# Performance work log

Hardware: AMD Instinct MI355X
Metric: run time of the kernel (lower is better)

## Reference

```python
import jax, jax.numpy as jnp
import numpy as np

HEAD, D_MODEL, D_KV = 16, 1024, 64
B, NQ, NK = 2, 2048, 2048


def setup_inputs() -> dict:
    key = jax.random.key(0)
    ks = jax.random.split(key, 10)
    s = 1.0 / np.sqrt(D_MODEL)
    return {
        "queries": jax.random.normal(ks[0], (B, NQ, D_MODEL), jnp.float32),
        "keys": jax.random.normal(ks[1], (B, NK, D_MODEL), jnp.float32),
        "values": jax.random.normal(ks[2], (B, NK, D_MODEL), jnp.float32),
        "group_prob": jax.random.uniform(ks[3], (B, 1, NQ, NK), jnp.float32),
        "attention_mask": jnp.ones((B, NK), jnp.int32),
        "Wq": jax.random.normal(ks[4], (D_MODEL, HEAD * D_KV), jnp.float32) * s,
        "bq": jnp.zeros((HEAD * D_KV,), jnp.float32),
        "Wk": jax.random.normal(ks[5], (D_MODEL, HEAD * D_KV), jnp.float32) * s,
        "bk": jnp.zeros((HEAD * D_KV,), jnp.float32),
        "Wv": jax.random.normal(ks[6], (D_MODEL, HEAD * D_KV), jnp.float32) * s,
        "bv": jnp.zeros((HEAD * D_KV,), jnp.float32),
    }


def reference(queries, keys, values, group_prob, attention_mask, Wq, bq, Wk, bk, Wv, bv):
    b_s, nq, _ = queries.shape
    nk = keys.shape[1]
    # projections -> [b, h, n, d]
    q = (queries @ Wq + bq).reshape(b_s, nq, HEAD, D_KV).transpose(0, 2, 1, 3)
    k = (keys @ Wk + bk).reshape(b_s, nk, HEAD, D_KV).transpose(0, 2, 1, 3)
    v = (values @ Wv + bv).reshape(b_s, nk, HEAD, D_KV).transpose(0, 2, 1, 3)
    att = jnp.einsum("bhqd,bhkd->bhqk", q, k) / np.sqrt(D_KV).astype(np.float32)
    # NOTE: original uses non-in-place `att.masked_fill(...)` and discards the
    # result, so attention_mask has NO effect on the computation. Replicated.
    att = jax.nn.softmax(att, axis=-1)
    att = att * group_prob  # post-softmax group gating, broadcast over heads
    out = jnp.einsum("bhqk,bhkd->bhqd", att, v)
    return out.transpose(0, 2, 1, 3).reshape(b_s, nq, D_MODEL)
```

## Files before the change

### kernel.cpp

```cpp
#include <hip/hip_runtime.h>
#include <hip/hip_bf16.h>
#include <cstdint>

typedef unsigned short ushort_t;
typedef __attribute__((ext_vector_type(8))) short short8;
typedef __attribute__((ext_vector_type(4))) float floatx4;
typedef __attribute__((ext_vector_type(4))) unsigned short ushort4_t;

#define H_   16
#define DKV_ 64
#define DM_  1024
#define B_   2
#define NQ_  2048
#define NK_  2048

__device__ __forceinline__ unsigned short f2bf(float f) {
  union { float f; unsigned int u; } v; v.f = f;
  unsigned int u = v.u;
  return (unsigned short)((u + 0x7fffu + ((u >> 16) & 1u)) >> 16);
}

__device__ __forceinline__ float fexp2(float x) { return __builtin_amdgcn_exp2f(x); }
__device__ __forceinline__ float frcp(float x)  { return __builtin_amdgcn_rcpf(x); }

__device__ __forceinline__ floatx4 mfma16(short8 a, short8 b, floatx4 c) {
  return __builtin_amdgcn_mfma_f32_16x16x32_bf16(a, b, c, 0, 0, 0);
}

__device__ __forceinline__ void gload_lds16(const ushort_t* g, ushort_t* l) {
  __builtin_amdgcn_global_load_lds(
      (const __attribute__((address_space(1))) void*)g,
      (__attribute__((address_space(3))) void*)l, 16, 0, 0);
}

__global__ __launch_bounds__(256) void cast_x_kernel(
    const float* __restrict__ q, const float* __restrict__ k,
    const float* __restrict__ v, ushort_t* __restrict__ dst)
{
  const int t = blockIdx.y;
  const float* src = (t == 0) ? q : (t == 1) ? k : v;
  ushort_t* d = dst + (size_t)t * 4096 * 1024;
  const int gid = blockIdx.x * 256 + threadIdx.x;
  #pragma unroll
  for (int u = 0; u < 8; u++) {
    const int i4 = u * 131072 + gid;
    floatx4 f = ((const floatx4*)src)[i4];
    ushort4_t o;
    #pragma unroll
    for (int e = 0; e < 4; e++) o[e] = f2bf(f[e]);
    *(ushort4_t*)&d[(size_t)i4 * 4] = o;
  }
}

__global__ __launch_bounds__(256) void cast_wt_kernel(
    const float* __restrict__ Wq, const float* __restrict__ Wk,
    const float* __restrict__ Wv, ushort_t* __restrict__ WtAll)
{
  __shared__ ushort_t tile[32][33];
  const int t = blockIdx.z;
  const float* W = (t == 0) ? Wq : (t == 1) ? Wk : Wv;
  ushort_t* Wt = WtAll + (size_t)t * 1024 * 1024;
  const int n0 = blockIdx.x * 32, k0 = blockIdx.y * 32;
  const int tid = threadIdx.x, r = tid >> 3, c4 = (tid & 7) * 4;
  floatx4 f = *(const floatx4*)&W[(size_t)(k0 + r) * 1024 + n0 + c4];
  #pragma unroll
  for (int e = 0; e < 4; e++) tile[r][c4 + e] = f2bf(f[e]);
  __syncthreads();
  ushort4_t o;
  #pragma unroll
  for (int e = 0; e < 4; e++) o[e] = tile[c4 + e][r];
  *(ushort4_t*)&Wt[(size_t)(n0 + r) * 1024 + k0 + c4] = o;
}

__global__ __launch_bounds__(256, 2) void proj_kernel2(
    const ushort_t* __restrict__ Xbf, const ushort_t* __restrict__ WtAll,
    const float* __restrict__ bq, const float* __restrict__ bk,
    const float* __restrict__ bv,
    ushort_t* __restrict__ Qb, ushort_t* __restrict__ Kb, ushort_t* __restrict__ Vt)
{
  const int mode = blockIdx.z;
  const ushort_t* X  = Xbf  + (size_t)mode * 4096 * 1024;
  const ushort_t* Wt = WtAll + (size_t)mode * 1024 * 1024;
  const float* bias  = (mode == 0) ? bq : (mode == 1) ? bk : bv;
  ushort_t* dst      = (mode == 0) ? Qb : (mode == 1) ? Kb : Vt;

  __shared__ ushort_t SM[8192];
  ushort_t* SA = SM;
  ushort_t* SB = SM + 4096;

  const int tid = threadIdx.x, lane = tid & 63, wid = tid >> 6;
  const int c = lane & 15, g = lane >> 4;
  const int m0 = blockIdx.y * 128, n0 = blockIdx.x * 128;
  const int wm = wid & 1, wn = wid >> 1, mb = wm * 64, nb = wn * 64;
  const int srow = lane >> 2;
  const int schunk = (lane & 3) * 8;

  floatx4 acc[4][4];
  #pragma unroll
  for (int i = 0; i < 4; i++)
    #pragma unroll
    for (int j = 0; j < 4; j++) acc[i][j] = floatx4{0.f, 0.f, 0.f, 0.f};

  for (int k0 = 0; k0 < DM_; k0 += 32) {
    __syncthreads();
    #pragma unroll
    for (int u = 0; u < 2; u++) {
      const int t = wid * 2 + u;
      gload_lds16(&X [(size_t)(m0 + t * 16 + srow) * 1024 + k0 + schunk], &SA[t * 512]);
      gload_lds16(&Wt[(size_t)(n0 + t * 16 + srow) * 1024 + k0 + schunk], &SB[t * 512]);
    }
    __syncthreads();

    short8 af[4], bfr[4];
    #pragma unroll
    for (int i = 0; i < 4; i++) af[i]  = *(const short8*)&SA[(mb + i * 16 + c) * 32 + g * 8];
    #pragma unroll
    for (int j = 0; j < 4; j++) bfr[j] = *(const short8*)&SB[(nb + j * 16 + c) * 32 + g * 8];
    #pragma unroll
    for (int i = 0; i < 4; i++)
      #pragma unroll
      for (int j = 0; j < 4; j++) acc[i][j] = mfma16(af[i], bfr[j], acc[i][j]);
  }

  __syncthreads();
  const float scale = (mode == 0) ? 0.18033688011112042f : 1.0f;
  ushort_t* EP = SM + wid * 2048;
  const int hh = (n0 + nb) >> 6;

  if (mode != 2) {
    for (int jj = 0; jj < 2; jj++) {
      #pragma unroll
      for (int jt = 0; jt < 2; jt++) {
        const int j = jj * 2 + jt;
        const float bb = bias[n0 + nb + j * 16 + c];
        #pragma unroll
        for (int i = 0; i < 4; i++)
          #pragma unroll
          for (int r = 0; r < 4; r++)
            EP[(i * 16 + g * 4 + r) * 32 + jt * 16 + c] =
                f2bf((acc[i][j][r] + bb) * scale);
      }
      #pragma unroll
      for (int u = 0; u < 8; u++) {
        const int rowl = u * 8 + (lane >> 3);
        ushort4_t vv = *(ushort4_t*)&EP[rowl * 32 + (lane & 7) * 4];
        const int rowg = m0 + mb + rowl;
        const int bb2 = rowg >> 11, nn = rowg & 2047;
        *(ushort4_t*)&dst[((size_t)(bb2 * H_ + hh) * NQ_ + nn) * DKV_ +
                          jj * 32 + (lane & 7) * 4] = vv;
      }
    }
  } else {
    const int bb2 = (m0 + mb) >> 11, nloc = (m0 + mb) & 2047;
    for (int j = 0; j < 4; j++) {
      const float bb = bias[n0 + nb + j * 16 + c];
      #pragma unroll
      for (int i = 0; i < 4; i++) {
        ushort4_t pk;
        #pragma unroll
        for (int r = 0; r < 4; r++) pk[r] = f2bf(acc[i][j][r] + bb);
        *(ushort4_t*)&EP[c * 72 + i * 16 + g * 4] = pk;
      }
      const int d0 = j * 16;
      #pragma unroll
      for (int u = 0; u < 2; u++) {
        const int coll = u * 8 + (lane >> 3);
        short8 vv = *(const short8*)&EP[coll * 72 + (lane & 7) * 8];
        *(short8*)&dst[((size_t)(bb2 * H_ + hh) * DKV_ + d0 + coll) * NK_ +
                       nloc + (lane & 7) * 8] = vv;
      }
    }
  }
}

constexpr int LDT = 40;
__global__ __launch_bounds__(256, 2) void proj_kernel_fb(
    const float* __restrict__ Xq, const float* __restrict__ Xk, const float* __restrict__ Xv,
    const float* __restrict__ Wq, const float* __restrict__ Wk, const float* __restrict__ Wv,
    const float* __restrict__ bq, const float* __restrict__ bk, const float* __restrict__ bv,
    ushort_t* __restrict__ Qb, ushort_t* __restrict__ Kb, ushort_t* __restrict__ Vt)
{
  const int mode = blockIdx.z;
  const float* X    = (mode == 0) ? Xq : (mode == 1) ? Xk : Xv;
  const float* W    = (mode == 0) ? Wq : (mode == 1) ? Wk : Wv;
  const float* bias = (mode == 0) ? bq : (mode == 1) ? bk : bv;
  ushort_t* dst     = (mode == 0) ? Qb : (mode == 1) ? Kb : Vt;

  __shared__ ushort_t Asm[128 * LDT];
  __shared__ ushort_t Bsm[128 * LDT];

  const int tid = threadIdx.x, lane = tid & 63, wid = tid >> 6;
  const int m0 = blockIdx.y * 128, n0 = blockIdx.x * 128;
  const int c = lane & 15, g = lane >> 4;
  const int wm = wid & 1, wn = wid >> 1, mb = wm * 64, nb = wn * 64;

  floatx4 acc[4][4];
  #pragma unroll
  for (int i = 0; i < 4; i++)
    #pragma unroll
    for (int j = 0; j < 4; j++) acc[i][j] = floatx4{0.f, 0.f, 0.f, 0.f};

  const int ar = tid >> 1, ah = tid & 1;
  const int bn = tid & 127, bh2 = tid >> 7;

  for (int k0 = 0; k0 < DM_; k0 += 32) {
    const floatx4* ap = (const floatx4*)(X + (size_t)(m0 + ar) * DM_ + k0 + ah * 16);
    floatx4 av0 = ap[0], av1 = ap[1], av2 = ap[2], av3 = ap[3];
    const float* wp = W + (size_t)(k0 + bh2 * 16) * 1024 + n0 + bn;
    float wv[16];
    #pragma unroll
    for (int j = 0; j < 16; j++) wv[j] = wp[j * 1024];
    short8 pa0, pa1, pb0, pb1;
    #pragma unroll
    for (int j = 0; j < 4; j++) {
      pa0[j] = (short)f2bf(av0[j]); pa0[4 + j] = (short)f2bf(av1[j]);
      pa1[j] = (short)f2bf(av2[j]); pa1[4 + j] = (short)f2bf(av3[j]);
    }
    #pragma unroll
    for (int j = 0; j < 8; j++) { pb0[j] = (short)f2bf(wv[j]); pb1[j] = (short)f2bf(wv[8 + j]); }
    __syncthreads();
    *(short8*)&Asm[ar * LDT + ah * 16]      = pa0;
    *(short8*)&Asm[ar * LDT + ah * 16 + 8]  = pa1;
    *(short8*)&Bsm[bn * LDT + bh2 * 16]     = pb0;
    *(short8*)&Bsm[bn * LDT + bh2 * 16 + 8] = pb1;
    __syncthreads();
    short8 af[4], bfr[4];
    #pragma unroll
    for (int i = 0; i < 4; i++) af[i]  = *(const short8*)&Asm[(mb + i * 16 + c) * LDT + g * 8];
    #pragma unroll
    for (int j = 0; j < 4; j++) bfr[j] = *(const short8*)&Bsm[(nb + j * 16 + c) * LDT + g * 8];
    #pragma unroll
    for (int i = 0; i < 4; i++)
      #pragma unroll
      for (int j = 0; j < 4; j++) acc[i][j] = mfma16(af[i], bfr[j], acc[i][j]);
  }
  #pragma unroll
  for (int j = 0; j < 4; j++) {
    const int col = n0 + nb + j * 16 + c;
    const float bv_ = bias[col];
    const int h = col >> 6, d = col & 63;
    #pragma unroll
    for (int i = 0; i < 4; i++)
      #pragma unroll
      for (int r = 0; r < 4; r++) {
        const int row = m0 + mb + i * 16 + g * 4 + r;
        const int b = row >> 11, n = row & 2047;
        float v = acc[i][j][r] + bv_;
        if (mode == 0) {
          v *= 0.18033688011112042f;
          dst[((size_t)(b * H_ + h) * NQ_ + n) * DKV_ + d] = f2bf(v);
        } else if (mode == 1) {
          dst[((size_t)(b * H_ + h) * NQ_ + n) * DKV_ + d] = f2bf(v);
        } else {
          dst[((size_t)(b * H_ + h) * DKV_ + d) * NK_ + n] = f2bf(v);
        }
      }
  }
}

__global__ __launch_bounds__(512, 4) void attn_kernel(
    const ushort_t* __restrict__ Qb, const ushort_t* __restrict__ Kb,
    const ushort_t* __restrict__ Vt, const float* __restrict__ gp,
    float* __restrict__ out)
{
  __shared__ ushort_t Ks[2][64 * 72];
  __shared__ ushort_t Vs[2][64 * 72];
  __shared__ ushort_t Pl[8][16 * 72];

  const int tid = threadIdx.x, lane = tid & 63, wid = tid >> 6;
  const int c = lane & 15, g = lane >> 4;
  const int h = blockIdx.x, b = blockIdx.z;
  const int bh = b * H_ + h;
  const int qw = blockIdx.y * 128 + wid * 16;

  const ushort_t* Qp = Qb + (size_t)bh * NQ_ * DKV_;
  const ushort_t* Kp = Kb + (size_t)bh * NK_ * DKV_;
  const ushort_t* Vp = Vt + (size_t)bh * DKV_ * NK_;
  const float* gpp = gp + (size_t)b * NQ_ * NK_ + (size_t)qw * NK_;
  ushort_t* Pw = Pl[wid];

  const int gx16 = (g >> 1) << 4;
  const int prd  = g ^ (((c >> 3) & 1) << 1);

  const int srow = tid >> 3;
  const int scol = (tid & 7) * 8;

  short8 qf[2];
  #pragma unroll
  for (int kc = 0; kc < 2; kc++)
    qf[kc] = *(const short8*)&Qp[(qw + c) * DKV_ + kc * 32 + g * 8];

  *(short8*)&Ks[0][srow * 72 + scol] = *(const short8*)&Kp[(size_t)srow * DKV_ + scol];
  *(short8*)&Vs[0][srow * 72 + scol] = *(const short8*)&Vp[(size_t)srow * NK_ + scol];
  __syncthreads();

  floatx4 o[4];
  float l[4];
  #pragma unroll
  for (int jd = 0; jd < 4; jd++) o[jd] = floatx4{0.f, 0.f, 0.f, 0.f};
  #pragma unroll
  for (int r = 0; r < 4; r++) l[r] = 0.f;

  for (int t = 0; t < NK_ / 64; t++) {
    const int k0 = t * 64;
    const int cur = t & 1, nxt = cur ^ 1;

    float gpv[4][4];
    #pragma unroll
    for (int r = 0; r < 4; r++) {
      const float* gq = gpp + (size_t)(g * 4 + r) * NK_ + k0 + c;
      #pragma unroll
      for (int jk = 0; jk < 4; jk++) gpv[jk][r] = gq[jk * 16];
    }

    short8 knx, vnx;
    const bool has_next = (t + 1) < NK_ / 64;
    if (has_next) {
      const int k1 = k0 + 64;
      knx = *(const short8*)&Kp[(size_t)(k1 + srow) * DKV_ + scol];
      vnx = *(const short8*)&Vp[(size_t)srow * NK_ + k1 + scol];
    }

    floatx4 s[4];
    #pragma unroll
    for (int jk = 0; jk < 4; jk++) s[jk] = floatx4{0.f, 0.f, 0.f, 0.f};
    #pragma unroll
    for (int jk = 0; jk < 4; jk++)
      #pragma unroll
      for (int kc = 0; kc < 2; kc++) {
        short8 kf = *(const short8*)&Ks[cur][(jk * 16 + c) * 72 + kc * 32 + g * 8];
        s[jk] = mfma16(qf[kc], kf, s[jk]);
      }

    #pragma unroll
    for (int jk = 0; jk < 4; jk++) {
      const int colw = (jk << 4) ^ gx16;
      #pragma unroll
      for (int r = 0; r < 4; r++) {
        const float p = fexp2(s[jk][r]);
        l[r] += p;
        Pw[(g * 4 + r) * 72 + colw + c] = f2bf(p * gpv[jk][r]);
      }
    }

    #pragma unroll
    for (int kc = 0; kc < 2; kc++) {
      short8 af = *(const short8*)&Pw[c * 72 + kc * 32 + prd * 8];
      #pragma unroll
      for (int jd = 0; jd < 4; jd++) {
        short8 vf = *(const short8*)&Vs[cur][(jd * 16 + c) * 72 + kc * 32 + g * 8];
        o[jd] = mfma16(af, vf, o[jd]);
      }
    }

    if (has_next) {
      *(short8*)&Ks[nxt][srow * 72 + scol] = knx;
      *(short8*)&Vs[nxt][srow * 72 + scol] = vnx;
    }
    __syncthreads();
  }

  float invl[4];
  #pragma unroll
  for (int r = 0; r < 4; r++) {
    float rs = l[r];
    rs += __shfl_xor(rs, 1);
    rs += __shfl_xor(rs, 2);
    rs += __shfl_xor(rs, 4);
    rs += __shfl_xor(rs, 8);
    invl[r] = frcp(rs);
  }
  #pragma unroll
  for (int jd = 0; jd < 4; jd++)
    #pragma unroll
    for (int r = 0; r < 4; r++) {
      const int row = qw + g * 4 + r;
      out[(size_t)(b * NQ_ + row) * 1024 + h * 64 + jd * 16 + c] =
          o[jd][r] * invl[r];
    }
}

extern "C" void kernel_launch(void* const* d_in, const int* in_sizes, int n_in,
                              void* d_out, int out_size, void* d_ws, size_t ws_size,
                              hipStream_t stream) {
  const float* queries = (const float*)d_in[0];
  const float* keys    = (const float*)d_in[1];
  const float* values  = (const float*)d_in[2];
  const float* gp      = (const float*)d_in[3];
  const float* Wq = (const float*)d_in[5];
  const float* bq = (const float*)d_in[6];
  const float* Wk = (const float*)d_in[7];
  const float* bk = (const float*)d_in[8];
  const float* Wv = (const float*)d_in[9];
  const float* bv = (const float*)d_in[10];

  const size_t SZ_QKV = (size_t)3 * B_ * H_ * NQ_ * DKV_;
  const size_t SZ_X   = (size_t)3 * 4096 * 1024;
  const size_t SZ_W   = (size_t)3 * 1024 * 1024;
  const size_t NEED   = (SZ_QKV + SZ_X + SZ_W) * sizeof(ushort_t);

  ushort_t* Qb = (ushort_t*)d_ws;
  ushort_t* Kb = Qb + (size_t)B_ * H_ * NQ_ * DKV_;
  ushort_t* Vt = Kb + (size_t)B_ * H_ * NK_ * DKV_;
  float* out = (float*)d_out;

  if (ws_size >= NEED) {
    ushort_t* Xbf = Qb + SZ_QKV;
    ushort_t* Wt  = Xbf + SZ_X;
    cast_x_kernel<<<dim3(512, 3), 256, 0, stream>>>(queries, keys, values, Xbf);
    cast_wt_kernel<<<dim3(32, 32, 3), 256, 0, stream>>>(Wq, Wk, Wv, Wt);
    proj_kernel2<<<dim3(8, 32, 3), 256, 0, stream>>>(
        Xbf, Wt, bq, bk, bv, Qb, Kb, Vt);
  } else {
    proj_kernel_fb<<<dim3(8, 32, 3), 256, 0, stream>>>(
        queries, keys, values, Wq, Wk, Wv, bq, bk, bv, Qb, Kb, Vt);
  }
  attn_kernel<<<dim3(H_, NQ_ / 128, B_), 512, 0, stream>>>(Qb, Kb, Vt, gp, out);
}
```

Baseline: 247.8 us.

## Compute transposed S so P stays in registers, skipping LDS round-trip

Swaps the MFMA operand order so each lane holds the scores of one query row across four consecutive keys. The softmax probabilities can then be packed straight into the A-operand of the PV MFMA with v_cvt_pk_bf16, and the per-wave P buffer in LDS goes away. To match that key ordering, V tiles are written to LDS with a permuted column layout, and group_prob is read as float4 vectors. This removes LDS writes and reads plus the scalar bf16 rounding, at the cost of split V stores and extra shuffles for the row sums.

```diff
diff --git a/kernel.cpp b/kernel.cpp
--- a/kernel.cpp
+++ b/kernel.cpp
@@ -4,7 +4,9 @@
 
 typedef unsigned short ushort_t;
 typedef __attribute__((ext_vector_type(8))) short short8;
+typedef __attribute__((ext_vector_type(4))) short short4v;
 typedef __attribute__((ext_vector_type(4))) float floatx4;
+typedef __attribute__((ext_vector_type(4))) unsigned int uintx4;
 typedef __attribute__((ext_vector_type(4))) unsigned short ushort4_t;
 
 #define H_   16
@@ -22,6 +24,12 @@
 
 __device__ __forceinline__ float fexp2(float x) { return __builtin_amdgcn_exp2f(x); }
 __device__ __forceinline__ float frcp(float x)  { return __builtin_amdgcn_rcpf(x); }
+
+__device__ __forceinline__ unsigned int cvt_pk_bf16(float lo, float hi) {
+  unsigned int r;
+  asm("v_cvt_pk_bf16_f32 %0, %1, %2" : "=v"(r) : "v"(lo), "v"(hi));
+  return r;
+}
 
 __device__ __forceinline__ floatx4 mfma16(short8 a, short8 b, floatx4 c) {
   return __builtin_amdgcn_mfma_f32_16x16x32_bf16(a, b, c, 0, 0, 0);
@@ -265,7 +273,6 @@
 {
   __shared__ ushort_t Ks[2][64 * 72];
   __shared__ ushort_t Vs[2][64 * 72];
-  __shared__ ushort_t Pl[8][16 * 72];
 
   const int tid = threadIdx.x, lane = tid & 63, wid = tid >> 6;
   const int c = lane & 15, g = lane >> 4;
@@ -276,14 +283,13 @@
   const ushort_t* Qp = Qb + (size_t)bh * NQ_ * DKV_;
   const ushort_t* Kp = Kb + (size_t)bh * NK_ * DKV_;
   const ushort_t* Vp = Vt + (size_t)bh * DKV_ * NK_;
-  const float* gpp = gp + (size_t)b * NQ_ * NK_ + (size_t)qw * NK_;
-  ushort_t* Pw = Pl[wid];
-
-  const int gx16 = (g >> 1) << 4;
-  const int prd  = g ^ (((c >> 3) & 1) << 1);
+  const float* gpq = gp + (size_t)b * NQ_ * NK_ + (size_t)(qw + c) * NK_;
 
   const int srow = tid >> 3;
-  const int scol = (tid & 7) * 8;
+  const int u    = tid & 7;
+  const int scol = u * 8;
+  const int so_lo = 32 * (u >> 2) + 8 * ((2 * u) & 3) + 4 * ((u >> 1) & 1);
+  const int so_hi = 32 * (u >> 2) + 8 * ((2 * u + 1) & 3) + 4 * ((u >> 1) & 1);
 
   short8 qf[2];
   #pragma unroll
@@ -291,61 +297,69 @@
     qf[kc] = *(const short8*)&Qp[(qw + c) * DKV_ + kc * 32 + g * 8];
 
   *(short8*)&Ks[0][srow * 72 + scol] = *(const short8*)&Kp[(size_t)srow * DKV_ + scol];
-  *(short8*)&Vs[0][srow * 72 + scol] = *(const short8*)&Vp[(size_t)srow * NK_ + scol];
+  {
+    short8 v8 = *(const short8*)&Vp[(size_t)srow * NK_ + scol];
+    short4v vlo, vhi;
+    #pragma unroll
+    for (int e = 0; e < 4; e++) { vlo[e] = v8[e]; vhi[e] = v8[4 + e]; }
+    *(short4v*)&Vs[0][srow * 72 + so_lo] = vlo;
+    *(short4v*)&Vs[0][srow * 72 + so_hi] = vhi;
+  }
   __syncthreads();
 
   floatx4 o[4];
-  float l[4];
+  float l = 0.f;
   #pragma unroll
   for (int jd = 0; jd < 4; jd++) o[jd] = floatx4{0.f, 0.f, 0.f, 0.f};
-  #pragma unroll
-  for (int r = 0; r < 4; r++) l[r] = 0.f;
 
   for (int t = 0; t < NK_ / 64; t++) {
     const int k0 = t * 64;
     const int cur = t & 1, nxt = cur ^ 1;
 
-    float gpv[4][4];
-    #pragma unroll
-    for (int r = 0; r < 4; r++) {
-      const float* gq = gpp + (size_t)(g * 4 + r) * NK_ + k0 + c;
-      #pragma unroll
-      for (int jk = 0; jk < 4; jk++) gpv[jk][r] = gq[jk * 16];
-    }
-
-    short8 knx, vnx;
+    floatx4 gpv[4];
+    #pragma unroll
+    for (int jk = 0; jk < 4; jk++)
+      gpv[jk] = *(const floatx4*)&gpq[k0 + jk * 16 + g * 4];
+
+    short8 knx;
+    short4v vlo, vhi;
     const bool has_next = (t + 1) < NK_ / 64;
     if (has_next) {
       const int k1 = k0 + 64;
       knx = *(const short8*)&Kp[(size_t)(k1 + srow) * DKV_ + scol];
-      vnx = *(const short8*)&Vp[(size_t)srow * NK_ + k1 + scol];
+      short8 v8 = *(const short8*)&Vp[(size_t)srow * NK_ + k1 + scol];
+      #pragma unroll
+      for (int e = 0; e < 4; e++) { vlo[e] = v8[e]; vhi[e] = v8[4 + e]; }
     }
 
     floatx4 s[4];
     #pragma unroll
-    for (int jk = 0; jk < 4; jk++) s[jk] = floatx4{0.f, 0.f, 0.f, 0.f};
-    #pragma unroll
-    for (int jk = 0; jk < 4; jk++)
+    for (int jk = 0; jk < 4; jk++) {
+      s[jk] = floatx4{0.f, 0.f, 0.f, 0.f};
       #pragma unroll
       for (int kc = 0; kc < 2; kc++) {
         short8 kf = *(const short8*)&Ks[cur][(jk * 16 + c) * 72 + kc * 32 + g * 8];
-        s[jk] = mfma16(qf[kc], kf, s[jk]);
-      }
-
+        s[jk] = mfma16(kf, qf[kc], s[jk]);
+      }
+    }
+
+    uintx4 afw[2];
     #pragma unroll
     for (int jk = 0; jk < 4; jk++) {
-      const int colw = (jk << 4) ^ gx16;
-      #pragma unroll
-      for (int r = 0; r < 4; r++) {
-        const float p = fexp2(s[jk][r]);
-        l[r] += p;
-        Pw[(g * 4 + r) * 72 + colw + c] = f2bf(p * gpv[jk][r]);
-      }
+      const float p0 = fexp2(s[jk][0]);
+      const float p1 = fexp2(s[jk][1]);
+      const float p2 = fexp2(s[jk][2]);
+      const float p3 = fexp2(s[jk][3]);
+      l += (p0 + p1) + (p2 + p3);
+      const unsigned int w0 = cvt_pk_bf16(p0 * gpv[jk][0], p1 * gpv[jk][1]);
+      const unsigned int w1 = cvt_pk_bf16(p2 * gpv[jk][2], p3 * gpv[jk][3]);
+      afw[jk >> 1][2 * (jk & 1) + 0] = w0;
+      afw[jk >> 1][2 * (jk & 1) + 1] = w1;
     }
 
     #pragma unroll
     for (int kc = 0; kc < 2; kc++) {
-      short8 af = *(const short8*)&Pw[c * 72 + kc * 32 + prd * 8];
+      const short8 af = __builtin_bit_cast(short8, afw[kc]);
       #pragma unroll
       for (int jd = 0; jd < 4; jd++) {
         short8 vf = *(const short8*)&Vs[cur][(jd * 16 + c) * 72 + kc * 32 + g * 8];
@@ -355,28 +369,27 @@
 
     if (has_next) {
       *(short8*)&Ks[nxt][srow * 72 + scol] = knx;
-      *(short8*)&Vs[nxt][srow * 72 + scol] = vnx;
+      *(short4v*)&Vs[nxt][srow * 72 + so_lo] = vlo;
+      *(short4v*)&Vs[nxt][srow * 72 + so_hi] = vhi;
     }
     __syncthreads();
   }
 
-  float invl[4];
-  #pragma unroll
-  for (int r = 0; r < 4; r++) {
-    float rs = l[r];
-    rs += __shfl_xor(rs, 1);
-    rs += __shfl_xor(rs, 2);
-    rs += __shfl_xor(rs, 4);
-    rs += __shfl_xor(rs, 8);
-    invl[r] = frcp(rs);
-  }
+  float lf = l;
+  lf += __shfl_xor(lf, 16);
+  lf += __shfl_xor(lf, 32);
+  const float inv = frcp(lf);
+  float invr[4];
+  #pragma unroll
+  for (int r = 0; r < 4; r++) invr[r] = __shfl(inv, g * 4 + r);
+
   #pragma unroll
   for (int jd = 0; jd < 4; jd++)
     #pragma unroll
     for (int r = 0; r < 4; r++) {
       const int row = qw + g * 4 + r;
       out[(size_t)(b * NQ_ + row) * 1024 + h * 64 + jd * 16 + c] =
-          o[jd][r] * invl[r];
+          o[jd][r] * invr[r];
     }
 }
 
```

Result: slower. 255.1 us (+2.9%).

## Give each attention wave two 16-row query tiles to reuse K/V fragments

Applied to the files above, without the earlier changes.

Each wave in the attention kernel now handles 32 query rows as two 16-row MFMA tiles, so every K and V fragment read from LDS feeds two MFMAs. The block shrinks from 512 to 256 threads and each thread stages two 8-element chunks of K and V per tile. This cuts LDS reads per MFMA and halves the number of barrier participants, but doubles the accumulator and score registers per thread and lowers the wave count per block, which may reduce latency hiding for the group_prob loads.

```diff
diff --git a/kernel.cpp b/kernel.cpp
--- a/kernel.cpp
+++ b/kernel.cpp
@@ -258,20 +258,20 @@
   }
 }
 
-__global__ __launch_bounds__(512, 4) void attn_kernel(
+__global__ __launch_bounds__(256, 2) void attn_kernel(
     const ushort_t* __restrict__ Qb, const ushort_t* __restrict__ Kb,
     const ushort_t* __restrict__ Vt, const float* __restrict__ gp,
     float* __restrict__ out)
 {
   __shared__ ushort_t Ks[2][64 * 72];
   __shared__ ushort_t Vs[2][64 * 72];
-  __shared__ ushort_t Pl[8][16 * 72];
+  __shared__ ushort_t Pl[4][32 * 72];
 
   const int tid = threadIdx.x, lane = tid & 63, wid = tid >> 6;
   const int c = lane & 15, g = lane >> 4;
   const int h = blockIdx.x, b = blockIdx.z;
   const int bh = b * H_ + h;
-  const int qw = blockIdx.y * 128 + wid * 16;
+  const int qw = blockIdx.y * 128 + wid * 32;
 
   const ushort_t* Qp = Qb + (size_t)bh * NQ_ * DKV_;
   const ushort_t* Kp = Kb + (size_t)bh * NK_ * DKV_;
@@ -282,102 +282,125 @@
   const int gx16 = (g >> 1) << 4;
   const int prd  = g ^ (((c >> 3) & 1) << 1);
 
-  const int srow = tid >> 3;
-  const int scol = (tid & 7) * 8;
-
-  short8 qf[2];
-  #pragma unroll
-  for (int kc = 0; kc < 2; kc++)
-    qf[kc] = *(const short8*)&Qp[(qw + c) * DKV_ + kc * 32 + g * 8];
-
-  *(short8*)&Ks[0][srow * 72 + scol] = *(const short8*)&Kp[(size_t)srow * DKV_ + scol];
-  *(short8*)&Vs[0][srow * 72 + scol] = *(const short8*)&Vp[(size_t)srow * NK_ + scol];
+  const int srow = tid >> 2;
+  const int scol = (tid & 3) * 8;
+
+  short8 qf[2][2];
+  #pragma unroll
+  for (int qh = 0; qh < 2; qh++)
+    #pragma unroll
+    for (int kc = 0; kc < 2; kc++)
+      qf[qh][kc] = *(const short8*)&Qp[(qw + qh * 16 + c) * DKV_ + kc * 32 + g * 8];
+
+  *(short8*)&Ks[0][srow * 72 + scol]      = *(const short8*)&Kp[(size_t)srow * DKV_ + scol];
+  *(short8*)&Ks[0][srow * 72 + scol + 32] = *(const short8*)&Kp[(size_t)srow * DKV_ + scol + 32];
+  *(short8*)&Vs[0][srow * 72 + scol]      = *(const short8*)&Vp[(size_t)srow * NK_ + scol];
+  *(short8*)&Vs[0][srow * 72 + scol + 32] = *(const short8*)&Vp[(size_t)srow * NK_ + scol + 32];
   __syncthreads();
 
-  floatx4 o[4];
-  float l[4];
-  #pragma unroll
-  for (int jd = 0; jd < 4; jd++) o[jd] = floatx4{0.f, 0.f, 0.f, 0.f};
-  #pragma unroll
-  for (int r = 0; r < 4; r++) l[r] = 0.f;
+  floatx4 o[2][4];
+  float l[2][4];
+  #pragma unroll
+  for (int qh = 0; qh < 2; qh++) {
+    #pragma unroll
+    for (int jd = 0; jd < 4; jd++) o[qh][jd] = floatx4{0.f, 0.f, 0.f, 0.f};
+    #pragma unroll
+    for (int r = 0; r < 4; r++) l[qh][r] = 0.f;
+  }
 
   for (int t = 0; t < NK_ / 64; t++) {
     const int k0 = t * 64;
     const int cur = t & 1, nxt = cur ^ 1;
 
-    float gpv[4][4];
-    #pragma unroll
-    for (int r = 0; r < 4; r++) {
-      const float* gq = gpp + (size_t)(g * 4 + r) * NK_ + k0 + c;
-      #pragma unroll
-      for (int jk = 0; jk < 4; jk++) gpv[jk][r] = gq[jk * 16];
-    }
-
-    short8 knx, vnx;
+    float gpv[2][4][4];
+    #pragma unroll
+    for (int qh = 0; qh < 2; qh++)
+      #pragma unroll
+      for (int r = 0; r < 4; r++) {
+        const float* gq = gpp + (size_t)(qh * 16 + g * 4 + r) * NK_ + k0 + c;
+        #pragma unroll
+        for (int jk = 0; jk < 4; jk++) gpv[qh][jk][r] = gq[jk * 16];
+      }
+
+    short8 knx0, knx1, vnx0, vnx1;
     const bool has_next = (t + 1) < NK_ / 64;
     if (has_next) {
       const int k1 = k0 + 64;
-      knx = *(const short8*)&Kp[(size_t)(k1 + srow) * DKV_ + scol];
-      vnx = *(const short8*)&Vp[(size_t)srow * NK_ + k1 + scol];
-    }
-
-    floatx4 s[4];
-    #pragma unroll
-    for (int jk = 0; jk < 4; jk++) s[jk] = floatx4{0.f, 0.f, 0.f, 0.f};
+      knx0 = *(const short8*)&Kp[(size_t)(k1 + srow) * DKV_ + scol];
+      knx1 = *(const short8*)&Kp[(size_t)(k1 + srow) * DKV_ + scol + 32];
+      vnx0 = *(const short8*)&Vp[(size_t)srow * NK_ + k1 + scol];
+      vnx1 = *(const short8*)&Vp[(size_t)srow * NK_ + k1 + scol + 32];
+    }
+
+    floatx4 s[2][4];
+    #pragma unroll
+    for (int qh = 0; qh < 2; qh++)
+      #pragma unroll
+      for (int jk = 0; jk < 4; jk++) s[qh][jk] = floatx4{0.f, 0.f, 0.f, 0.f};
     #pragma unroll
     for (int jk = 0; jk < 4; jk++)
       #pragma unroll
       for (int kc = 0; kc < 2; kc++) {
         short8 kf = *(const short8*)&Ks[cur][(jk * 16 + c) * 72 + kc * 32 + g * 8];
-        s[jk] = mfma16(qf[kc], kf, s[jk]);
-      }
-
-    #pragma unroll
-    for (int jk = 0; jk < 4; jk++) {
-      const int colw = (jk << 4) ^ gx16;
-      #pragma unroll
-      for (int r = 0; r < 4; r++) {
-        const float p = fexp2(s[jk][r]);
-        l[r] += p;
-        Pw[(g * 4 + r) * 72 + colw + c] = f2bf(p * gpv[jk][r]);
-      }
-    }
+        s[0][jk] = mfma16(qf[0][kc], kf, s[0][jk]);
+        s[1][jk] = mfma16(qf[1][kc], kf, s[1][jk]);
+      }
+
+    #pragma unroll
+    for (int qh = 0; qh < 2; qh++)
+      #pragma unroll
+      for (int jk = 0; jk < 4; jk++) {
+        const int colw = (jk << 4) ^ gx16;
+        #pragma unroll
+        for (int r = 0; r < 4; r++) {
+          const float p = fexp2(s[qh][jk][r]);
+          l[qh][r] += p;
+          Pw[(qh * 16 + g * 4 + r) * 72 + colw + c] = f2bf(p * gpv[qh][jk][r]);
+        }
+      }
 
     #pragma unroll
     for (int kc = 0; kc < 2; kc++) {
-      short8 af = *(const short8*)&Pw[c * 72 + kc * 32 + prd * 8];
+      short8 af0 = *(const short8*)&Pw[(c) * 72 + kc * 32 + prd * 8];
+      short8 af1 = *(const short8*)&Pw[(16 + c) * 72 + kc * 32 + prd * 8];
       #pragma unroll
       for (int jd = 0; jd < 4; jd++) {
         short8 vf = *(const short8*)&Vs[cur][(jd * 16 + c) * 72 + kc * 32 + g * 8];
-        o[jd] = mfma16(af, vf, o[jd]);
+        o[0][jd] = mfma16(af0, vf, o[0][jd]);
+        o[1][jd] = mfma16(af1, vf, o[1][jd]);
       }
     }
 
     if (has_next) {
-      *(short8*)&Ks[nxt][srow * 72 + scol] = knx;
-      *(short8*)&Vs[nxt][srow * 72 + scol] = vnx;
+      *(short8*)&Ks[nxt][srow * 72 + scol]      = knx0;
+      *(short8*)&Ks[nxt][srow * 72 + scol + 32] = knx1;
+      *(short8*)&Vs[nxt][srow * 72 + scol]      = vnx0;
+      *(short8*)&Vs[nxt][srow * 72 + scol + 32] = vnx1;
     }
     __syncthreads();
   }
 
-  float invl[4];
-  #pragma unroll
-  for (int r = 0; r < 4; r++) {
-    float rs = l[r];
-    rs += __shfl_xor(rs, 1);
-    rs += __shfl_xor(rs, 2);
-    rs += __shfl_xor(rs, 4);
-    rs += __shfl_xor(rs, 8);
-    invl[r] = frcp(rs);
-  }
-  #pragma unroll
-  for (int jd = 0; jd < 4; jd++)
+  #pragma unroll
+  for (int qh = 0; qh < 2; qh++) {
+    float invl[4];
     #pragma unroll
     for (int r = 0; r < 4; r++) {
-      const int row = qw + g * 4 + r;
-      out[(size_t)(b * NQ_ + row) * 1024 + h * 64 + jd * 16 + c] =
-          o[jd][r] * invl[r];
-    }
+      float rs = l[qh][r];
+      rs += __shfl_xor(rs, 1);
+      rs += __shfl_xor(rs, 2);
+      rs += __shfl_xor(rs, 4);
+      rs += __shfl_xor(rs, 8);
+      invl[r] = frcp(rs);
+    }
+    #pragma unroll
+    for (int jd = 0; jd < 4; jd++)
+      #pragma unroll
+      for (int r = 0; r < 4; r++) {
+        const int row = qw + qh * 16 + g * 4 + r;
+        out[(size_t)(b * NQ_ + row) * 1024 + h * 64 + jd * 16 + c] =
+            o[qh][jd][r] * invl[r];
+      }
+  }
 }
 
 extern "C" void kernel_launch(void* const* d_in, const int* in_sizes, int n_in,
@@ -415,5 +438,5 @@
     proj_kernel_fb<<<dim3(8, 32, 3), 256, 0, stream>>>(
         queries, keys, values, Wq, Wk, Wv, bq, bk, bv, Qb, Kb, Vt);
   }
-  attn_kernel<<<dim3(H_, NQ_ / 128, B_), 512, 0, stream>>>(Qb, Kb, Vt, gp, out);
-}
+  attn_kernel<<<dim3(H_, NQ_ / 128, B_), 256, 0, stream>>>(Qb, Kb, Vt, gp, out);
+}
```

Measured after the change: 253.7 us. +2.4%, slower.
